# Kernel optimization log

Hardware: AMD Instinct MI355X
Metric: run time of the kernel (lower is better)

## Reference

```python
import jax, jax.numpy as jnp
import numpy as np

N, E, D, H, C, B, P = 100_000, 1_600_000, 128, 128, 64, 8, 0.2


def setup_inputs() -> dict:
    key = jax.random.key(0)
    ks = jax.random.split(key, 16)
    sc = 1.0 / np.sqrt(D).astype(np.float32)
    return {
        "x": jax.random.normal(ks[0], (N, D), jnp.float32),
        "query": jax.random.normal(ks[1], (B, D), jnp.float32),
        "batch": jnp.sort(jax.random.randint(ks[2], (N,), 0, B)),
        "edge_index": jax.random.randint(ks[3], (2, E), 0, N),
        "W0": jax.random.normal(ks[4], (D, H), jnp.float32) * sc,
        "b0": jnp.zeros((H,), jnp.float32),
        "W1": jax.random.normal(ks[5], (H, H), jnp.float32) * sc,
        "b1": jnp.zeros((H,), jnp.float32),
        "W2": jax.random.normal(ks[6], (H, H), jnp.float32) * sc,
        "b2": jnp.zeros((H,), jnp.float32),
        "W3": jax.random.normal(ks[7], (H, H), jnp.float32) * sc,
        "b3": jnp.zeros((H,), jnp.float32),
        "Wc": jax.random.normal(ks[8], (H, C), jnp.float32) * sc,
        "bc": jnp.zeros((C,), jnp.float32),
    }


def _gcn_norm(edge_index, n, dtype):
    # PyG gcn_norm with self-loops: A_hat = D^-1/2 (A+I) D^-1/2
    loop = jnp.arange(n)
    fs = jnp.concatenate([edge_index[0], loop])  # source of each (edge+loop)
    fd = jnp.concatenate([edge_index[1], loop])  # target (aggregation index)
    deg = jax.ops.segment_sum(jnp.ones(fs.shape[0], dtype), fd, num_segments=n)
    dis = jnp.where(deg > 0, jax.lax.rsqrt(deg), jnp.zeros_like(deg))
    return fs, fd, dis[fs] * dis[fd]


def reference(x, query, batch, edge_index, W0, b0, W1, b1, W2, b2, W3, b3, Wc, bc):
    n = x.shape[0]
    fs, fd, norm = _gcn_norm(edge_index, n, x.dtype)

    def conv(h, W, b):
        hw = h @ W  # [N,H]
        agg = jax.ops.segment_sum(hw[fs] * norm[:, None], fd, num_segments=n)
        return agg + b

    h = query[batch] * x  # broadcast graph query onto its nodes
    res = h
    for W, b in ((W0, b0), (W1, b1), (W2, b2)):
        h = jax.nn.relu(conv(h, W, b) + res)
        res = h
    h = conv(h, W3, b3) + res
    out = h @ Wc + bc
    # dropout (training=True, p=0.2) with fixed key for determinism
    keep = jax.random.bernoulli(jax.random.key(42), 1.0 - P, out.shape)
    return jnp.where(keep, out / (1.0 - P), jnp.zeros_like(out))
```

## Files before the change

### kernel.cpp

```cpp
#include <hip/hip_runtime.h>
#include <cstdint>
#include <cstddef>


typedef short bf16x8 __attribute__((ext_vector_type(8)));
typedef float f32x4 __attribute__((ext_vector_type(4)));

static __device__ __forceinline__ uint32_t f2bf(float x) {
  uint32_t u = __float_as_uint(x);
  return (u + 0x7fffu + ((u >> 16) & 1u)) >> 16;
}
static __device__ __forceinline__ uint32_t pack2(float a, float b) {
  return f2bf(a) | (f2bf(b) << 16);
}
static __device__ __forceinline__ float bf_lo(uint32_t u) { return __uint_as_float(u << 16); }
static __device__ __forceinline__ float bf_hi(uint32_t u) { return __uint_as_float(u & 0xffff0000u); }

static __device__ __forceinline__ uint32_t rotl32(uint32_t v, int d) {
  return (v << d) | (v >> (32 - d));
}

static __device__ __forceinline__ void threefry2x32(uint32_t k0, uint32_t k1,
                                                    uint32_t& x0, uint32_t& x1) {
  uint32_t k2 = k0 ^ k1 ^ 0x1BD11BDAu;
  x0 += k0; x1 += k1;
#define TF_R(r) { x0 += x1; x1 = rotl32(x1, (r)); x1 ^= x0; }
  TF_R(13) TF_R(15) TF_R(26) TF_R(6)
  x0 += k1; x1 += k2 + 1u;
  TF_R(17) TF_R(29) TF_R(16) TF_R(24)
  x0 += k2; x1 += k0 + 2u;
  TF_R(13) TF_R(15) TF_R(26) TF_R(6)
  x0 += k0; x1 += k1 + 3u;
  TF_R(17) TF_R(29) TF_R(16) TF_R(24)
  x0 += k1; x1 += k2 + 4u;
  TF_R(13) TF_R(15) TF_R(26) TF_R(6)
  x0 += k2; x1 += k0 + 5u;
#undef TF_R
}

__global__ void init_kernel(int* cnt, int n) {
  int i = blockIdx.x * blockDim.x + threadIdx.x;
  if (i < n) cnt[i] = 0;
}

__global__ void pre_kernel(const int* __restrict__ fd, int* __restrict__ cnt,
                           int* __restrict__ rank, int e, int eb,
                           const float* __restrict__ x, const float* __restrict__ query,
                           const int* __restrict__ batch, uint32_t* __restrict__ hb,
                           int n) {
  int b = blockIdx.x;
  if (b < eb) {
    int i = b * 256 + threadIdx.x;
    if (i < e) rank[i] = atomicAdd(&cnt[fd[i]], 1);
  } else {
    int i = (b - eb) * 256 + threadIdx.x;
    int total = n * 64;
    if (i < total) {
      int node = i >> 6;
      int w = i & 63;
      int bq = batch[node];
      float2 xv = ((const float2*)x)[i];
      float2 qv = ((const float2*)query)[bq * 64 + w];
      hb[i] = pack2(xv.x * qv.x, xv.y * qv.y);
    }
  }
}

__global__ void scanA_kernel(const int* __restrict__ cnt, int* __restrict__ off,
                             int* __restrict__ bsum, int n) {
  __shared__ int s[256];
  int t = threadIdx.x;
  int i = blockIdx.x * 256 + t;
  int v = (i < n) ? cnt[i] : 0;
  s[t] = v;
  __syncthreads();
  for (int d = 1; d < 256; d <<= 1) {
    int add = (t >= d) ? s[t - d] : 0;
    __syncthreads();
    s[t] += add;
    __syncthreads();
  }
  if (i < n) off[i] = s[t] - v;
  if (t == 255) bsum[blockIdx.x] = s[255];
}

__global__ void scanB_kernel(const int* __restrict__ bsum, int* __restrict__ boff,
                             int nb, int* __restrict__ off, int n) {
  __shared__ int s[512];
  int t = threadIdx.x;
  int v = (t < nb) ? bsum[t] : 0;
  s[t] = v;
  __syncthreads();
  for (int d = 1; d < 512; d <<= 1) {
    int add = (t >= d) ? s[t - d] : 0;
    __syncthreads();
    s[t] += add;
    __syncthreads();
  }
  if (t < nb) boff[t] = s[t] - v;
  if (t == nb - 1) off[n] = s[t];
}

__global__ void scanC_kernel(int* __restrict__ off, const int* __restrict__ boff,
                             const int* __restrict__ cnt, float* __restrict__ dis, int n) {
  int i = blockIdx.x * 256 + threadIdx.x;
  if (i < n) {
    off[i] += boff[blockIdx.x];
    dis[i] = 1.0f / sqrtf((float)(cnt[i] + 1));
  }
}

__global__ void fill_kernel(const int* __restrict__ fs, const int* __restrict__ fd,
                            const int* __restrict__ rank, const int* __restrict__ off,
                            const float* __restrict__ dis,
                            uint32_t* __restrict__ csr, int e) {
  int i = blockIdx.x * blockDim.x + threadIdx.x;
  if (i < e) {
    int s = fs[i], d = fd[i];
    uint32_t w15 = f2bf(dis[s] * dis[d]) & 0x7fffu;
    csr[off[d] + rank[i]] = (uint32_t)s | (w15 << 17);
  }
}

template<int BN, int OUT_MODE, int WSPLIT>
__global__ __launch_bounds__(256)
void mfma_gemm_kernel(const uint32_t* __restrict__ Abf,
                      const float* __restrict__ Wm,
                      const float* __restrict__ bias,
                      void* __restrict__ Cout, int nrows) {
  constexpr int CT = BN / 16;
  __shared__ short Wt[WSPLIT][BN][136];
  const int tid = threadIdx.x;

  for (int q = tid; q < (128 * BN) / 4; q += 256) {
    int el = q * 4;
    int k = el / BN;
    int col = el % BN;
    float4 w4 = *(const float4*)(Wm + el);
    float wv[4] = {w4.x, w4.y, w4.z, w4.w};
#pragma unroll
    for (int j = 0; j < 4; ++j) {
      uint32_t hi = f2bf(wv[j]);
      Wt[0][col + j][k] = (short)hi;
      if constexpr (WSPLIT == 2) {
        float hif = __uint_as_float(hi << 16);
        Wt[1][col + j][k] = (short)f2bf(wv[j] - hif);
      }
    }
  }
  __syncthreads();

  const int wave = tid >> 6;
  const int lane = tid & 63;
  const int lrow = lane & 15;
  const int lk = lane >> 4;
  const int rowbase = blockIdx.x * 256 + wave * 64;
  const uint16_t* Au = (const uint16_t*)Abf;

  f32x4 acc[4][CT];
#pragma unroll
  for (int rt = 0; rt < 4; ++rt)
#pragma unroll
    for (int ct = 0; ct < CT; ++ct) acc[rt][ct] = (f32x4){0.f, 0.f, 0.f, 0.f};

#pragma unroll
  for (int s = 0; s < 4; ++s) {
    bf16x8 a[4];
#pragma unroll
    for (int rt = 0; rt < 4; ++rt) {
      int gr = rowbase + rt * 16 + lrow;
      int gra = (gr < nrows) ? gr : 0;
      a[rt] = *reinterpret_cast<const bf16x8*>(Au + (size_t)gra * 128 + s * 32 + lk * 8);
    }
#pragma unroll
    for (int ct = 0; ct < CT; ++ct) {
      bf16x8 bhi = *reinterpret_cast<const bf16x8*>(&Wt[0][ct * 16 + lrow][s * 32 + lk * 8]);
#pragma unroll
      for (int rt = 0; rt < 4; ++rt)
        acc[rt][ct] = __builtin_amdgcn_mfma_f32_16x16x32_bf16(a[rt], bhi, acc[rt][ct], 0, 0, 0);
      if constexpr (WSPLIT == 2) {
        bf16x8 blo = *reinterpret_cast<const bf16x8*>(&Wt[1][ct * 16 + lrow][s * 32 + lk * 8]);
#pragma unroll
        for (int rt = 0; rt < 4; ++rt)
          acc[rt][ct] = __builtin_amdgcn_mfma_f32_16x16x32_bf16(a[rt], blo, acc[rt][ct], 0, 0, 0);
      }
    }
  }

#pragma unroll
  for (int rt = 0; rt < 4; ++rt)
#pragma unroll
    for (int ct = 0; ct < CT; ++ct)
#pragma unroll
      for (int r = 0; r < 4; ++r) {
        int gr = rowbase + rt * 16 + lk * 4 + r;
        if (gr >= nrows) continue;
        int col = ct * 16 + lrow;
        float v = acc[rt][ct][r];
        if constexpr (OUT_MODE == 1) {
          uint32_t pk = __builtin_amdgcn_cvt_pk_fp8_f32(v, v, 0u, false);
          ((uint8_t*)Cout)[(size_t)gr * BN + col] = (uint8_t)pk;
        } else {
          v += bias[col];
          uint32_t x0 = 0u, x1 = (uint32_t)gr * (uint32_t)BN + (uint32_t)col;
          threefry2x32(0u, 42u, x0, x1);
          uint32_t bits = x0 ^ x1;
          float u = __uint_as_float((bits >> 9) | 0x3F800000u) - 1.0f;
          ((float*)Cout)[(size_t)gr * BN + col] = (u < 0.8f) ? (v / 0.8f) : 0.0f;
        }
      }
}

#define CVT4(acc0, acc1, acc2, acc3, w, word)                                  \
  acc0 = fmaf(w, __builtin_amdgcn_cvt_f32_fp8((word), 0), acc0);               \
  acc1 = fmaf(w, __builtin_amdgcn_cvt_f32_fp8((word), 1), acc1);               \
  acc2 = fmaf(w, __builtin_amdgcn_cvt_f32_fp8((word), 2), acc2);               \
  acc3 = fmaf(w, __builtin_amdgcn_cvt_f32_fp8((word), 3), acc3);

#define EDGE_ACC(cw, R)                                                        \
  {                                                                            \
    float w = __uint_as_float(((cw) >> 17) << 16);                             \
    CVT4(acc[0], acc[1], acc[2], acc[3], w, (R).x)                             \
    CVT4(acc[4], acc[5], acc[6], acc[7], w, (R).y)                             \
    CVT4(acc[8], acc[9], acc[10], acc[11], w, (R).z)                           \
    CVT4(acc[12], acc[13], acc[14], acc[15], w, (R).w)                         \
  }

__global__ __launch_bounds__(256)
void agg_kernel(const uint8_t* __restrict__ hw8, uint32_t* __restrict__ hb,
                const float* __restrict__ bias,
                const int* __restrict__ off, const uint32_t* __restrict__ csr,
                const float* __restrict__ dis, int relu, int n) {
  const int v = (blockIdx.x * blockDim.x + threadIdx.x) >> 3;
  const int sl = threadIdx.x & 7;
  if (v >= n) return;

  const int eoff = sl * 16;
  float dv = dis[v];
  float sw = dv * dv;
  uint4 selfw = *(const uint4*)(hw8 + (size_t)v * 128 + eoff);
  uint4 resA = *(const uint4*)(hb + (size_t)v * 64 + sl * 8);
  uint4 resB = *(const uint4*)(hb + (size_t)v * 64 + sl * 8 + 4);
  const float* bb = bias + eoff;

  float acc[16];
  acc[0]  = bb[0]  + bf_lo(resA.x);
  acc[1]  = bb[1]  + bf_hi(resA.x);
  acc[2]  = bb[2]  + bf_lo(resA.y);
  acc[3]  = bb[3]  + bf_hi(resA.y);
  acc[4]  = bb[4]  + bf_lo(resA.z);
  acc[5]  = bb[5]  + bf_hi(resA.z);
  acc[6]  = bb[6]  + bf_lo(resA.w);
  acc[7]  = bb[7]  + bf_hi(resA.w);
  acc[8]  = bb[8]  + bf_lo(resB.x);
  acc[9]  = bb[9]  + bf_hi(resB.x);
  acc[10] = bb[10] + bf_lo(resB.y);
  acc[11] = bb[11] + bf_hi(resB.y);
  acc[12] = bb[12] + bf_lo(resB.z);
  acc[13] = bb[13] + bf_hi(resB.z);
  acc[14] = bb[14] + bf_lo(resB.w);
  acc[15] = bb[15] + bf_hi(resB.w);
  CVT4(acc[0], acc[1], acc[2], acc[3], sw, selfw.x)
  CVT4(acc[4], acc[5], acc[6], acc[7], sw, selfw.y)
  CVT4(acc[8], acc[9], acc[10], acc[11], sw, selfw.z)
  CVT4(acc[12], acc[13], acc[14], acc[15], sw, selfw.w)

  const int s0 = off[v], s1 = off[v + 1];
  int i = s0;
  for (; i + 8 <= s1; i += 8) {
    uint32_t c[8];
    uint4 r[8];
#pragma unroll
    for (int j = 0; j < 8; ++j) c[j] = csr[i + j];
#pragma unroll
    for (int j = 0; j < 8; ++j)
      r[j] = *(const uint4*)(hw8 + (size_t)(c[j] & 0x1ffffu) * 128 + eoff);
    EDGE_ACC(c[0], r[0]) EDGE_ACC(c[1], r[1]) EDGE_ACC(c[2], r[2]) EDGE_ACC(c[3], r[3])
    EDGE_ACC(c[4], r[4]) EDGE_ACC(c[5], r[5]) EDGE_ACC(c[6], r[6]) EDGE_ACC(c[7], r[7])
  }
  if (i + 4 <= s1) {
    uint32_t c[4];
    uint4 r[4];
#pragma unroll
    for (int j = 0; j < 4; ++j) c[j] = csr[i + j];
#pragma unroll
    for (int j = 0; j < 4; ++j)
      r[j] = *(const uint4*)(hw8 + (size_t)(c[j] & 0x1ffffu) * 128 + eoff);
    EDGE_ACC(c[0], r[0]) EDGE_ACC(c[1], r[1]) EDGE_ACC(c[2], r[2]) EDGE_ACC(c[3], r[3])
    i += 4;
  }
  for (; i < s1; ++i) {
    uint32_t c = csr[i];
    uint4 r = *(const uint4*)(hw8 + (size_t)(c & 0x1ffffu) * 128 + eoff);
    EDGE_ACC(c, r)
  }

  if (relu) {
#pragma unroll
    for (int t = 0; t < 16; ++t) acc[t] = fmaxf(acc[t], 0.f);
  }
  uint4 oA, oB;
  oA.x = pack2(acc[0], acc[1]);
  oA.y = pack2(acc[2], acc[3]);
  oA.z = pack2(acc[4], acc[5]);
  oA.w = pack2(acc[6], acc[7]);
  oB.x = pack2(acc[8], acc[9]);
  oB.y = pack2(acc[10], acc[11]);
  oB.z = pack2(acc[12], acc[13]);
  oB.w = pack2(acc[14], acc[15]);
  *(uint4*)(hb + (size_t)v * 64 + sl * 8) = oA;
  *(uint4*)(hb + (size_t)v * 64 + sl * 8 + 4) = oB;
}
#undef EDGE_ACC
#undef CVT4

extern "C" void kernel_launch(void* const* d_in, const int* in_sizes, int n_in,
                              void* d_out, int out_size, void* d_ws, size_t ws_size,
                              hipStream_t stream) {
  const float* x     = (const float*)d_in[0];
  const float* query = (const float*)d_in[1];
  const int*   batch = (const int*)d_in[2];
  const int*   eidx  = (const int*)d_in[3];
  const float* W[4]  = {(const float*)d_in[4], (const float*)d_in[6],
                        (const float*)d_in[8], (const float*)d_in[10]};
  const float* bv[4] = {(const float*)d_in[5], (const float*)d_in[7],
                        (const float*)d_in[9], (const float*)d_in[11]};
  const float* Wc = (const float*)d_in[12];
  const float* bc = (const float*)d_in[13];
  float* out = (float*)d_out;

  const int n = in_sizes[2];
  const int e = in_sizes[3] / 2;
  const int* fs = eidx;
  const int* fd = eidx + e;

  char* p = (char*)d_ws;
  auto carve = [&](size_t bytes) -> void* {
    void* r = (void*)p;
    p += (bytes + 255) & ~(size_t)255;
    return r;
  };
  const int nscan = (n + 255) / 256;
  int*      cnt     = (int*)carve((size_t)n * 4);
  int*      off     = (int*)carve((size_t)(n + 1) * 4);
  int*      bsum    = (int*)carve((size_t)nscan * 4);
  int*      boff    = (int*)carve((size_t)nscan * 4);
  int*      rank    = (int*)carve((size_t)e * 4);
  float*    dis     = (float*)carve((size_t)n * 4);
  uint32_t* csr     = (uint32_t*)carve((size_t)e * 4);
  uint32_t* hb      = (uint32_t*)carve((size_t)n * 64 * 4);
  uint8_t*  hw8     = (uint8_t*)carve((size_t)n * 128);

  const int eb = (e + 255) / 256;
  const int h0b = (n * 64 + 255) / 256;

  init_kernel<<<nscan, 256, 0, stream>>>(cnt, n);
  pre_kernel<<<eb + h0b, 256, 0, stream>>>(fd, cnt, rank, e, eb, x, query, batch, hb, n);
  scanA_kernel<<<nscan, 256, 0, stream>>>(cnt, off, bsum, n);
  scanB_kernel<<<1, 512, 0, stream>>>(bsum, boff, nscan, off, n);
  scanC_kernel<<<nscan, 256, 0, stream>>>(off, boff, cnt, dis, n);
  fill_kernel<<<eb, 256, 0, stream>>>(fs, fd, rank, off, dis, csr, e);

  const int gblk = (n + 255) / 256;
  for (int l = 0; l < 4; ++l) {
    mfma_gemm_kernel<128, 1, 1><<<gblk, 256, 0, stream>>>(hb, W[l], nullptr, hw8, n);
    agg_kernel<<<(n * 8 + 255) / 256, 256, 0, stream>>>(hw8, hb, bv[l], off, csr,
                                                        dis, (l < 3) ? 1 : 0, n);
  }
  mfma_gemm_kernel<64, 0, 2><<<gblk, 256, 0, stream>>>(hb, Wc, bc, out, n);
}
```

Measured before the change: 406.5 us.

## Factor GCN normalization into source-side GEMM scaling and destination-side scaling

Splits the symmetric norm dis[s]*dis[d]: the GEMM epilogue scales each row by dis before the fp8 store, and aggregation sums neighbor rows unweighted, then applies dis[v] once at the end. The CSR now holds plain source indices instead of packed index+bf16 weight, so fill no longer gathers dis, and the per-edge FMA with a decoded weight becomes a plain add. Also replaces the init kernel with hipMemsetAsync and merges the degree-count and h0 computation into fewer blocks. The fp8 values now carry the dis-scaled magnitudes, which changes quantization slightly.

```diff
diff --git a/kernel.cpp b/kernel.cpp
--- a/kernel.cpp
+++ b/kernel.cpp
@@ -38,30 +38,24 @@
 #undef TF_R
 }
 
-__global__ void init_kernel(int* cnt, int n) {
-  int i = blockIdx.x * blockDim.x + threadIdx.x;
-  if (i < n) cnt[i] = 0;
-}
-
 __global__ void pre_kernel(const int* __restrict__ fd, int* __restrict__ cnt,
-                           int* __restrict__ rank, int e, int eb,
+                           int* __restrict__ rank, int e,
                            const float* __restrict__ x, const float* __restrict__ query,
                            const int* __restrict__ batch, uint32_t* __restrict__ hb,
                            int n) {
-  int b = blockIdx.x;
-  if (b < eb) {
-    int i = b * 256 + threadIdx.x;
-    if (i < e) rank[i] = atomicAdd(&cnt[fd[i]], 1);
-  } else {
-    int i = (b - eb) * 256 + threadIdx.x;
-    int total = n * 64;
-    if (i < total) {
-      int node = i >> 6;
-      int w = i & 63;
+  int i = blockIdx.x * 256 + threadIdx.x;
+  if (i < e) rank[i] = atomicAdd(&cnt[fd[i]], 1);
+  int total = n * 64;
+#pragma unroll
+  for (int j = 0; j < 4; ++j) {
+    int q = (blockIdx.x * 4 + j) * 256 + threadIdx.x;
+    if (q < total) {
+      int node = q >> 6;
+      int w = q & 63;
       int bq = batch[node];
-      float2 xv = ((const float2*)x)[i];
+      float2 xv = ((const float2*)x)[q];
       float2 qv = ((const float2*)query)[bq * 64 + w];
-      hb[i] = pack2(xv.x * qv.x, xv.y * qv.y);
+      hb[q] = pack2(xv.x * qv.x, xv.y * qv.y);
     }
   }
 }
@@ -112,14 +106,9 @@
 
 __global__ void fill_kernel(const int* __restrict__ fs, const int* __restrict__ fd,
                             const int* __restrict__ rank, const int* __restrict__ off,
-                            const float* __restrict__ dis,
-                            uint32_t* __restrict__ csr, int e) {
+                            int* __restrict__ csr, int e) {
   int i = blockIdx.x * blockDim.x + threadIdx.x;
-  if (i < e) {
-    int s = fs[i], d = fd[i];
-    uint32_t w15 = f2bf(dis[s] * dis[d]) & 0x7fffu;
-    csr[off[d] + rank[i]] = (uint32_t)s | (w15 << 17);
-  }
+  if (i < e) csr[off[fd[i]] + rank[i]] = fs[i];
 }
 
 template<int BN, int OUT_MODE, int WSPLIT>
@@ -127,6 +116,7 @@
 void mfma_gemm_kernel(const uint32_t* __restrict__ Abf,
                       const float* __restrict__ Wm,
                       const float* __restrict__ bias,
+                      const float* __restrict__ dis,
                       void* __restrict__ Cout, int nrows) {
   constexpr int CT = BN / 16;
   __shared__ short Wt[WSPLIT][BN][136];
@@ -198,6 +188,7 @@
         int col = ct * 16 + lrow;
         float v = acc[rt][ct][r];
         if constexpr (OUT_MODE == 1) {
+          v *= dis[gr];
           uint32_t pk = __builtin_amdgcn_cvt_pk_fp8_f32(v, v, 0u, false);
           ((uint8_t*)Cout)[(size_t)gr * BN + col] = (uint8_t)pk;
         } else {
@@ -211,25 +202,28 @@
       }
 }
 
-#define CVT4(acc0, acc1, acc2, acc3, w, word)                                  \
-  acc0 = fmaf(w, __builtin_amdgcn_cvt_f32_fp8((word), 0), acc0);               \
-  acc1 = fmaf(w, __builtin_amdgcn_cvt_f32_fp8((word), 1), acc1);               \
-  acc2 = fmaf(w, __builtin_amdgcn_cvt_f32_fp8((word), 2), acc2);               \
-  acc3 = fmaf(w, __builtin_amdgcn_cvt_f32_fp8((word), 3), acc3);
-
-#define EDGE_ACC(cw, R)                                                        \
+#define CVT4_SET(a0, a1, a2, a3, word)                                         \
+  a0 = __builtin_amdgcn_cvt_f32_fp8((word), 0);                                \
+  a1 = __builtin_amdgcn_cvt_f32_fp8((word), 1);                                \
+  a2 = __builtin_amdgcn_cvt_f32_fp8((word), 2);                                \
+  a3 = __builtin_amdgcn_cvt_f32_fp8((word), 3);
+#define CVT4_ADD(a0, a1, a2, a3, word)                                         \
+  a0 += __builtin_amdgcn_cvt_f32_fp8((word), 0);                               \
+  a1 += __builtin_amdgcn_cvt_f32_fp8((word), 1);                               \
+  a2 += __builtin_amdgcn_cvt_f32_fp8((word), 2);                               \
+  a3 += __builtin_amdgcn_cvt_f32_fp8((word), 3);
+#define EDGE_ACC(R)                                                            \
   {                                                                            \
-    float w = __uint_as_float(((cw) >> 17) << 16);                             \
-    CVT4(acc[0], acc[1], acc[2], acc[3], w, (R).x)                             \
-    CVT4(acc[4], acc[5], acc[6], acc[7], w, (R).y)                             \
-    CVT4(acc[8], acc[9], acc[10], acc[11], w, (R).z)                           \
-    CVT4(acc[12], acc[13], acc[14], acc[15], w, (R).w)                         \
+    CVT4_ADD(acc[0], acc[1], acc[2], acc[3], (R).x)                            \
+    CVT4_ADD(acc[4], acc[5], acc[6], acc[7], (R).y)                            \
+    CVT4_ADD(acc[8], acc[9], acc[10], acc[11], (R).z)                          \
+    CVT4_ADD(acc[12], acc[13], acc[14], acc[15], (R).w)                        \
   }
 
 __global__ __launch_bounds__(256)
 void agg_kernel(const uint8_t* __restrict__ hw8, uint32_t* __restrict__ hb,
                 const float* __restrict__ bias,
-                const int* __restrict__ off, const uint32_t* __restrict__ csr,
+                const int* __restrict__ off, const int* __restrict__ csr,
                 const float* __restrict__ dis, int relu, int n) {
   const int v = (blockIdx.x * blockDim.x + threadIdx.x) >> 3;
   const int sl = threadIdx.x & 7;
@@ -237,82 +231,82 @@
 
   const int eoff = sl * 16;
   float dv = dis[v];
-  float sw = dv * dv;
   uint4 selfw = *(const uint4*)(hw8 + (size_t)v * 128 + eoff);
+
+  float acc[16];
+  CVT4_SET(acc[0], acc[1], acc[2], acc[3], selfw.x)
+  CVT4_SET(acc[4], acc[5], acc[6], acc[7], selfw.y)
+  CVT4_SET(acc[8], acc[9], acc[10], acc[11], selfw.z)
+  CVT4_SET(acc[12], acc[13], acc[14], acc[15], selfw.w)
+
+  const int s0 = off[v], s1 = off[v + 1];
+  int i = s0;
+  for (; i + 8 <= s1; i += 8) {
+    int c[8];
+    uint4 r[8];
+#pragma unroll
+    for (int j = 0; j < 8; ++j) c[j] = csr[i + j];
+#pragma unroll
+    for (int j = 0; j < 8; ++j)
+      r[j] = *(const uint4*)(hw8 + (size_t)c[j] * 128 + eoff);
+    EDGE_ACC(r[0]) EDGE_ACC(r[1]) EDGE_ACC(r[2]) EDGE_ACC(r[3])
+    EDGE_ACC(r[4]) EDGE_ACC(r[5]) EDGE_ACC(r[6]) EDGE_ACC(r[7])
+  }
+  if (i + 4 <= s1) {
+    int c[4];
+    uint4 r[4];
+#pragma unroll
+    for (int j = 0; j < 4; ++j) c[j] = csr[i + j];
+#pragma unroll
+    for (int j = 0; j < 4; ++j)
+      r[j] = *(const uint4*)(hw8 + (size_t)c[j] * 128 + eoff);
+    EDGE_ACC(r[0]) EDGE_ACC(r[1]) EDGE_ACC(r[2]) EDGE_ACC(r[3])
+    i += 4;
+  }
+  for (; i < s1; ++i) {
+    uint4 r = *(const uint4*)(hw8 + (size_t)csr[i] * 128 + eoff);
+    EDGE_ACC(r)
+  }
+
   uint4 resA = *(const uint4*)(hb + (size_t)v * 64 + sl * 8);
   uint4 resB = *(const uint4*)(hb + (size_t)v * 64 + sl * 8 + 4);
   const float* bb = bias + eoff;
-
-  float acc[16];
-  acc[0]  = bb[0]  + bf_lo(resA.x);
-  acc[1]  = bb[1]  + bf_hi(resA.x);
-  acc[2]  = bb[2]  + bf_lo(resA.y);
-  acc[3]  = bb[3]  + bf_hi(resA.y);
-  acc[4]  = bb[4]  + bf_lo(resA.z);
-  acc[5]  = bb[5]  + bf_hi(resA.z);
-  acc[6]  = bb[6]  + bf_lo(resA.w);
-  acc[7]  = bb[7]  + bf_hi(resA.w);
-  acc[8]  = bb[8]  + bf_lo(resB.x);
-  acc[9]  = bb[9]  + bf_hi(resB.x);
-  acc[10] = bb[10] + bf_lo(resB.y);
-  acc[11] = bb[11] + bf_hi(resB.y);
-  acc[12] = bb[12] + bf_lo(resB.z);
-  acc[13] = bb[13] + bf_hi(resB.z);
-  acc[14] = bb[14] + bf_lo(resB.w);
-  acc[15] = bb[15] + bf_hi(resB.w);
-  CVT4(acc[0], acc[1], acc[2], acc[3], sw, selfw.x)
-  CVT4(acc[4], acc[5], acc[6], acc[7], sw, selfw.y)
-  CVT4(acc[8], acc[9], acc[10], acc[11], sw, selfw.z)
-  CVT4(acc[12], acc[13], acc[14], acc[15], sw, selfw.w)
-
-  const int s0 = off[v], s1 = off[v + 1];
-  int i = s0;
-  for (; i + 8 <= s1; i += 8) {
-    uint32_t c[8];
-    uint4 r[8];
-#pragma unroll
-    for (int j = 0; j < 8; ++j) c[j] = csr[i + j];
-#pragma unroll
-    for (int j = 0; j < 8; ++j)
-      r[j] = *(const uint4*)(hw8 + (size_t)(c[j] & 0x1ffffu) * 128 + eoff);
-    EDGE_ACC(c[0], r[0]) EDGE_ACC(c[1], r[1]) EDGE_ACC(c[2], r[2]) EDGE_ACC(c[3], r[3])
-    EDGE_ACC(c[4], r[4]) EDGE_ACC(c[5], r[5]) EDGE_ACC(c[6], r[6]) EDGE_ACC(c[7], r[7])
-  }
-  if (i + 4 <= s1) {
-    uint32_t c[4];
-    uint4 r[4];
-#pragma unroll
-    for (int j = 0; j < 4; ++j) c[j] = csr[i + j];
-#pragma unroll
-    for (int j = 0; j < 4; ++j)
-      r[j] = *(const uint4*)(hw8 + (size_t)(c[j] & 0x1ffffu) * 128 + eoff);
-    EDGE_ACC(c[0], r[0]) EDGE_ACC(c[1], r[1]) EDGE_ACC(c[2], r[2]) EDGE_ACC(c[3], r[3])
-    i += 4;
-  }
-  for (; i < s1; ++i) {
-    uint32_t c = csr[i];
-    uint4 r = *(const uint4*)(hw8 + (size_t)(c & 0x1ffffu) * 128 + eoff);
-    EDGE_ACC(c, r)
-  }
-
+  float o[16];
+  o[0]  = fmaf(dv, acc[0],  bb[0]  + bf_lo(resA.x));
+  o[1]  = fmaf(dv, acc[1],  bb[1]  + bf_hi(resA.x));
+  o[2]  = fmaf(dv, acc[2],  bb[2]  + bf_lo(resA.y));
+  o[3]  = fmaf(dv, acc[3],  bb[3]  + bf_hi(resA.y));
+  o[4]  = fmaf(dv, acc[4],  bb[4]  + bf_lo(resA.z));
+  o[5]  = fmaf(dv, acc[5],  bb[5]  + bf_hi(resA.z));
+  o[6]  = fmaf(dv, acc[6],  bb[6]  + bf_lo(resA.w));
+  o[7]  = fmaf(dv, acc[7],  bb[7]  + bf_hi(resA.w));
+  o[8]  = fmaf(dv, acc[8],  bb[8]  + bf_lo(resB.x));
+  o[9]  = fmaf(dv, acc[9],  bb[9]  + bf_hi(resB.x));
+  o[10] = fmaf(dv, acc[10], bb[10] + bf_lo(resB.y));
+  o[11] = fmaf(dv, acc[11], bb[11] + bf_hi(resB.y));
+  o[12] = fmaf(dv, acc[12], bb[12] + bf_lo(resB.z));
+  o[13] = fmaf(dv, acc[13], bb[13] + bf_hi(resB.z));
+  o[14] = fmaf(dv, acc[14], bb[14] + bf_lo(resB.w));
+  o[15] = fmaf(dv, acc[15], bb[15] + bf_hi(resB.w));
   if (relu) {
 #pragma unroll
-    for (int t = 0; t < 16; ++t) acc[t] = fmaxf(acc[t], 0.f);
+    for (int t = 0; t < 16; ++t) o[t] = fmaxf(o[t], 0.f);
   }
   uint4 oA, oB;
-  oA.x = pack2(acc[0], acc[1]);
-  oA.y = pack2(acc[2], acc[3]);
-  oA.z = pack2(acc[4], acc[5]);
-  oA.w = pack2(acc[6], acc[7]);
-  oB.x = pack2(acc[8], acc[9]);
-  oB.y = pack2(acc[10], acc[11]);
-  oB.z = pack2(acc[12], acc[13]);
-  oB.w = pack2(acc[14], acc[15]);
+  oA.x = pack2(o[0], o[1]);
+  oA.y = pack2(o[2], o[3]);
+  oA.z = pack2(o[4], o[5]);
+  oA.w = pack2(o[6], o[7]);
+  oB.x = pack2(o[8], o[9]);
+  oB.y = pack2(o[10], o[11]);
+  oB.z = pack2(o[12], o[13]);
+  oB.w = pack2(o[14], o[15]);
   *(uint4*)(hb + (size_t)v * 64 + sl * 8) = oA;
   *(uint4*)(hb + (size_t)v * 64 + sl * 8 + 4) = oB;
 }
 #undef EDGE_ACC
-#undef CVT4
+#undef CVT4_ADD
+#undef CVT4_SET
 
 extern "C" void kernel_launch(void* const* d_in, const int* in_sizes, int n_in,
                               void* d_out, int out_size, void* d_ws, size_t ws_size,
@@ -347,25 +341,26 @@
   int*      boff    = (int*)carve((size_t)nscan * 4);
   int*      rank    = (int*)carve((size_t)e * 4);
   float*    dis     = (float*)carve((size_t)n * 4);
-  uint32_t* csr     = (uint32_t*)carve((size_t)e * 4);
+  int*      csr     = (int*)carve((size_t)e * 4);
   uint32_t* hb      = (uint32_t*)carve((size_t)n * 64 * 4);
   uint8_t*  hw8     = (uint8_t*)carve((size_t)n * 128);
 
   const int eb = (e + 255) / 256;
-  const int h0b = (n * 64 + 255) / 256;
-
-  init_kernel<<<nscan, 256, 0, stream>>>(cnt, n);
-  pre_kernel<<<eb + h0b, 256, 0, stream>>>(fd, cnt, rank, e, eb, x, query, batch, hb, n);
+  const int h0b = (n * 64 + 1023) / 1024;
+  const int preb = (eb > h0b) ? eb : h0b;
+
+  hipMemsetAsync(cnt, 0, (size_t)n * 4, stream);
+  pre_kernel<<<preb, 256, 0, stream>>>(fd, cnt, rank, e, x, query, batch, hb, n);
   scanA_kernel<<<nscan, 256, 0, stream>>>(cnt, off, bsum, n);
   scanB_kernel<<<1, 512, 0, stream>>>(bsum, boff, nscan, off, n);
   scanC_kernel<<<nscan, 256, 0, stream>>>(off, boff, cnt, dis, n);
-  fill_kernel<<<eb, 256, 0, stream>>>(fs, fd, rank, off, dis, csr, e);
+  fill_kernel<<<eb, 256, 0, stream>>>(fs, fd, rank, off, csr, e);
 
   const int gblk = (n + 255) / 256;
   for (int l = 0; l < 4; ++l) {
-    mfma_gemm_kernel<128, 1, 1><<<gblk, 256, 0, stream>>>(hb, W[l], nullptr, hw8, n);
+    mfma_gemm_kernel<128, 1, 1><<<gblk, 256, 0, stream>>>(hb, W[l], nullptr, dis, hw8, n);
     agg_kernel<<<(n * 8 + 255) / 256, 256, 0, stream>>>(hw8, hb, bv[l], off, csr,
                                                         dis, (l < 3) ? 1 : 0, n);
   }
-  mfma_gemm_kernel<64, 0, 2><<<gblk, 256, 0, stream>>>(hb, Wc, bc, out, n);
-}
+  mfma_gemm_kernel<64, 0, 2><<<gblk, 256, 0, stream>>>(hb, Wc, bc, nullptr, out, n);
+}
```

Result: slower. 444.8 us (+9.4%).
